# Kernel tuning notes

Measured on AMD Instinct MI355X. Metric: run time of the kernel, lower is better.

The kernel has to match this reference:

```python
import jax, jax.numpy as jnp
import numpy as np

T = 4096       # sentence length
E = 256        # embedding_dim
H = 512        # hidden_dim (bidirectional total)
HD = H // 2    # per-direction hidden
V = 100000     # vocab_size
NT = 16        # tagset_size
START, STOP = 14, 15
NEG = -10000.0


def setup_inputs() -> dict:
    key = jax.random.key(0)
    ks = jax.random.split(key, 20)
    sentence = jax.random.randint(ks[0], (T,), 0, V)
    emb = jax.random.normal(ks[1], (V, E), dtype=jnp.float32)
    # PyTorch LSTM params: gate order [i, f, g, o], weight_ih [4*HD, E], weight_hh [4*HD, HD]
    s = 1.0 / np.sqrt(HD)
    def U(k, shape):
        return jax.random.uniform(k, shape, dtype=jnp.float32, minval=-s, maxval=s)
    Wih_f, Whh_f = U(ks[2], (4 * HD, E)), U(ks[3], (4 * HD, HD))
    bih_f, bhh_f = U(ks[4], (4 * HD,)), U(ks[5], (4 * HD,))
    Wih_b, Whh_b = U(ks[6], (4 * HD, E)), U(ks[7], (4 * HD, HD))
    bih_b, bhh_b = U(ks[8], (4 * HD,)), U(ks[9], (4 * HD,))
    h0 = jax.random.normal(ks[10], (2, 1, HD), dtype=jnp.float32)  # init_hidden()
    c0 = jax.random.normal(ks[11], (2, 1, HD), dtype=jnp.float32)
    # attention params (zeros in the original; small randn for a non-degenerate baseline)
    w_omega = jax.random.normal(ks[12], (H, H), dtype=jnp.float32) * 0.01
    u_omega = jax.random.normal(ks[13], (H,), dtype=jnp.float32) * 0.01
    sl = 1.0 / np.sqrt(H)
    W_tag = jax.random.uniform(ks[14], (NT, H), dtype=jnp.float32, minval=-sl, maxval=sl)
    b_tag = jax.random.uniform(ks[15], (NT,), dtype=jnp.float32, minval=-sl, maxval=sl)
    transitions = jax.random.normal(ks[16], (NT, NT), dtype=jnp.float32)
    transitions = transitions.at[START, :].set(NEG).at[:, STOP].set(NEG)
    return dict(sentence=sentence, emb=emb,
                Wih_f=Wih_f, Whh_f=Whh_f, bih_f=bih_f, bhh_f=bhh_f,
                Wih_b=Wih_b, Whh_b=Whh_b, bih_b=bih_b, bhh_b=bhh_b,
                h0=h0, c0=c0, w_omega=w_omega, u_omega=u_omega,
                W_tag=W_tag, b_tag=b_tag, transitions=transitions)


def _lstm_dir(x, h0, c0, Wih, Whh, bih, bhh, reverse):
    # x: [T, E]; returns hidden states [T, HD]
    def step(carry, xt):
        h, c = carry
        g = xt @ Wih.T + h @ Whh.T + bih + bhh  # [4*HD]
        i, f, gg, o = jnp.split(g, 4)
        i, f, o = jax.nn.sigmoid(i), jax.nn.sigmoid(f), jax.nn.sigmoid(o)
        c = f * c + i * jnp.tanh(gg)
        h = o * jnp.tanh(c)
        return (h, c), h
    _, hs = jax.lax.scan(step, (h0, c0), x, reverse=reverse)
    return hs


def _lstm_feats(sentence, emb, Wih_f, Whh_f, bih_f, bhh_f,
                Wih_b, Whh_b, bih_b, bhh_b, h0, c0,
                w_omega, u_omega, W_tag, b_tag):
    x = emb[sentence]  # [T, E]
    hf = _lstm_dir(x, h0[0, 0], c0[0, 0], Wih_f, Whh_f, bih_f, bhh_f, False)
    hb = _lstm_dir(x, h0[1, 0], c0[1, 0], Wih_b, Whh_b, bih_b, bhh_b, True)
    out = jnp.concatenate([hf, hb], axis=-1)  # [T, H] (lstm_out with batch=1 squeezed)
    # attention_net: softmax over time of a scalar score per position
    logits = jnp.tanh(out @ w_omega) @ u_omega  # [T]
    alphas = jax.nn.softmax(logits)
    attn_out = out * alphas[:, None]  # [T, H]
    return attn_out @ W_tag.T + b_tag  # [T, NT]


def _viterbi(feats, transitions):
    init = jnp.full((NT,), NEG, dtype=feats.dtype).at[START].set(0.0)
    def step(fv, feat):
        scores = fv[None, :] + transitions  # [next_tag, prev_tag]
        bp = jnp.argmax(scores, axis=1)
        return jnp.max(scores, axis=1) + feat, bp
    fv, bps = jax.lax.scan(step, init, feats)
    terminal = fv + transitions[STOP]
    best = jnp.argmax(terminal)
    score = terminal[best]
    def back(tag, bp):
        return bp[tag], tag
    _, path = jax.lax.scan(back, best, bps, reverse=True)  # path[t] = best tag at t
    return score, path


def reference(sentence, emb, Wih_f, Whh_f, bih_f, bhh_f,
              Wih_b, Whh_b, bih_b, bhh_b, h0, c0,
              w_omega, u_omega, W_tag, b_tag, transitions):
    feats = _lstm_feats(sentence, emb, Wih_f, Whh_f, bih_f, bhh_f,
                        Wih_b, Whh_b, bih_b, bhh_b, h0, c0,
                        w_omega, u_omega, W_tag, b_tag)
    score, path = _viterbi(feats, transitions)
    return score, path
```

## Files before the change

kernel.cpp:

```cpp
#include <hip/hip_runtime.h>
#include <hip/hip_fp16.h>

#define T_LEN 4096
#define START_TAG 14
#define STOP_TAG 15
#define NEG_VAL -10000.0f

typedef unsigned int u32;
typedef unsigned short u16;
typedef unsigned long long u64;
typedef int v4i __attribute__((ext_vector_type(4)));

#define GX_OFF      0u
#define OUT_OFF     16777216u
#define LOGITS_OFF  25165824u
#define ALPHAS_OFF  25182208u
#define FEATS_OFF   25198592u
#define CMAT_OFF    25460736u
#define VIN_OFF     25591808u
#define BP_OFF      25600000u
#define BMAP_OFF    25632768u
#define STAIL_OFF   25640960u
#define BEST_OFF    25649152u

__device__ __forceinline__ u32 packq(int q0, int q1, int q2, int q3) {
  return (u32)(q0 & 255) | ((u32)(q1 & 255) << 8) |
         ((u32)(q2 & 255) << 16) | ((u32)(q3 & 255) << 24);
}

__device__ __forceinline__ float sigm(float x) {
  return __builtin_amdgcn_rcpf(1.f + __expf(-x));
}
__device__ __forceinline__ float tanh_fast(float x) {
  float e = __expf(-2.f * fabsf(x));
  float r = (1.f - e) * __builtin_amdgcn_rcpf(1.f + e);
  return copysignf(r, x);
}

#if defined(__has_builtin)
#  if __has_builtin(__builtin_amdgcn_sdot4)
#    define DOT4(a, b, c) __builtin_amdgcn_sdot4((a), (b), (c), false)
#  endif
#endif
#ifndef DOT4
__device__ __forceinline__ int dot4_emu(int a, int b, int c) {
  #pragma unroll
  for (int j = 0; j < 4; ++j)
    c += (int)((signed char)(a >> (8 * j))) * (int)((signed char)(b >> (8 * j)));
  return c;
}
#  define DOT4(a, b, c) dot4_emu((a), (b), (c))
#endif

__device__ __forceinline__ void wg_barrier() {
  asm volatile("s_waitcnt lgkmcnt(0)" ::: "memory");
  __builtin_amdgcn_s_barrier();
  __builtin_amdgcn_sched_barrier(0);
}

__global__ void prep_kernel(float* logits) {
  const int i = threadIdx.x + blockIdx.x * 1024;
  if (i < 4096) logits[i] = 0.f;
}

__global__ __launch_bounds__(256) void gx_kernel(
    const int* __restrict__ sentence, const float* __restrict__ emb,
    const float* __restrict__ Wih_f, const float* __restrict__ Wih_b,
    const float* __restrict__ bih_f, const float* __restrict__ bhh_f,
    const float* __restrict__ bih_b, const float* __restrict__ bhh_b,
    __half* __restrict__ Gx)
{
  __shared__ float ws[32][260];
  const int r0 = blockIdx.x * 32;
  const int t0 = blockIdx.y * 32;
  const int tid = threadIdx.x;
  {
    const int c4 = (tid & 63) * 4;
    const int rA = tid >> 6;
    #pragma unroll
    for (int p = 0; p < 8; ++p) {
      const int rr = rA + p * 4;
      const int R = r0 + rr;
      const float* src = (R < 1024) ? (Wih_f + (size_t)R * 256 + c4)
                                    : (Wih_b + (size_t)(R - 1024) * 256 + c4);
      *(float4*)&ws[rr][c4] = *(const float4*)src;
    }
  }
  __syncthreads();
  const int ttb = tid >> 4, rgb = tid & 15;
  const int s0r = sentence[t0 + ttb];
  const int s1r = sentence[t0 + ttb + 16];
  const float* x0p = emb + (size_t)s0r * 256;
  const float* x1p = emb + (size_t)s1r * 256;
  float acc00 = 0, acc01 = 0, acc10 = 0, acc11 = 0;
  #pragma unroll 4
  for (int c4 = 0; c4 < 256; c4 += 4) {
    float4 x0 = *(const float4*)(x0p + c4);
    float4 x1 = *(const float4*)(x1p + c4);
    float4 w0 = *(const float4*)&ws[rgb][c4];
    float4 w1 = *(const float4*)&ws[rgb + 16][c4];
    acc00 += x0.x*w0.x + x0.y*w0.y + x0.z*w0.z + x0.w*w0.w;
    acc01 += x0.x*w1.x + x0.y*w1.y + x0.z*w1.z + x0.w*w1.w;
    acc10 += x1.x*w0.x + x1.y*w0.y + x1.z*w0.z + x1.w*w0.w;
    acc11 += x1.x*w1.x + x1.y*w1.y + x1.z*w1.z + x1.w*w1.w;
  }
  #pragma unroll
  for (int ri = 0; ri < 2; ++ri) {
    const int R = r0 + rgb + ri * 16;
    const int dir = R >> 10, grow = R & 1023;
    const int gate = grow >> 8, dd = grow & 255;
    const float bias = dir ? (bih_b[grow] + bhh_b[grow])
                           : (bih_f[grow] + bhh_f[grow]);
    const float a0 = ri ? acc01 : acc00;
    const float a1 = ri ? acc11 : acc10;
    const size_t off = (size_t)dir * 1024 + dd * 4 + gate;
    Gx[(size_t)(t0 + ttb) * 2048 + off]      = __float2half(a0 + bias);
    Gx[(size_t)(t0 + ttb + 16) * 2048 + off] = __float2half(a1 + bias);
  }
}

__global__ __launch_bounds__(512, 2) void lstm_kernel(
    const float* __restrict__ Whh_f, const float* __restrict__ Whh_b,
    const float* __restrict__ h0, const float* __restrict__ c0,
    const __half* __restrict__ Gx, float* __restrict__ out_lstm)
{
  const int dir = blockIdx.x;
  const int tid = threadIdx.x;
  const int w = tid >> 6, l = tid & 63;
  const float* Whh = dir ? Whh_b : Whh_f;

  __shared__ __align__(16) char hq8[2][256];
  __shared__ __align__(16) int graw[512];
  __shared__ float fsh[512];
  __shared__ __align__(16) u16 hist[128 * 256];

  if (w < 4) {
    const int mr = l & 15, q = l >> 4;
    v4i wfrag[8][4];
    #pragma unroll
    for (int m = 0; m < 8; ++m) {
      const int row = 128 * w + 16 * m + mr;
      const float* wr = Whh + (size_t)row * 256 + 16 * q;
      float mx = 1e-10f;
      #pragma unroll
      for (int t = 0; t < 4; ++t) {
        #pragma unroll
        for (int c4 = 0; c4 < 4; ++c4) {
          float4 f = *(const float4*)(wr + 64 * t + 4 * c4);
          mx = fmaxf(mx, fmaxf(fmaxf(fabsf(f.x), fabsf(f.y)),
                               fmaxf(fabsf(f.z), fabsf(f.w))));
        }
      }
      mx = fmaxf(mx, __shfl_xor(mx, 16));
      mx = fmaxf(mx, __shfl_xor(mx, 32));
      const float qs = 127.f / mx;
      if (q == 0) fsh[row] = mx * (1.f / (127.f * 32.f));
      #pragma unroll
      for (int t = 0; t < 4; ++t) {
        u32 pk[4];
        #pragma unroll
        for (int c4 = 0; c4 < 4; ++c4) {
          float4 f = *(const float4*)(wr + 64 * t + 4 * c4);
          pk[c4] = packq((int)rintf(f.x * qs), (int)rintf(f.y * qs),
                         (int)rintf(f.z * qs), (int)rintf(f.w * qs));
        }
        v4i v; v[0] = (int)pk[0]; v[1] = (int)pk[1]; v[2] = (int)pk[2]; v[3] = (int)pk[3];
        wfrag[m][t] = v;
      }
    }
    wg_barrier();

    for (int s = 0; s < T_LEN; ++s) {
      const char* hc = hq8[s & 1];
      v4i bfr[4];
      #pragma unroll
      for (int t = 0; t < 4; ++t)
        bfr[t] = *(const v4i*)(hc + 64 * t + 16 * q);
      #pragma unroll
      for (int m = 0; m < 8; ++m) {
        v4i acc; acc[0] = 0; acc[1] = 0; acc[2] = 0; acc[3] = 0;
        acc = __builtin_amdgcn_mfma_i32_16x16x64_i8(wfrag[m][0], bfr[0], acc, 0, 0, 0);
        acc = __builtin_amdgcn_mfma_i32_16x16x64_i8(wfrag[m][1], bfr[1], acc, 0, 0, 0);
        acc = __builtin_amdgcn_mfma_i32_16x16x64_i8(wfrag[m][2], bfr[2], acc, 0, 0, 0);
        acc = __builtin_amdgcn_mfma_i32_16x16x64_i8(wfrag[m][3], bfr[3], acc, 0, 0, 0);
        if (mr == 0)
          *(v4i*)&graw[128 * w + 16 * m + 4 * q] = acc;
      }
      wg_barrier();
      wg_barrier();
      if ((s & 127) == 127) {
        const int sbase = s - 127;
        #pragma unroll 4
        for (int i = 0; i < 16; ++i) {
          const int idx = tid + i * 512;
          const int step = idx >> 6, d0 = (idx & 63) * 4;
          const int tt = sbase + step;
          const int tg = dir ? (T_LEN - 1 - tt) : tt;
          uint2 hv = ((const uint2*)hist)[idx];
          float4 ov4;
          ov4.x = __half2float(__ushort_as_half((u16)(hv.x & 0xffff)));
          ov4.y = __half2float(__ushort_as_half((u16)(hv.x >> 16)));
          ov4.z = __half2float(__ushort_as_half((u16)(hv.y & 0xffff)));
          ov4.w = __half2float(__ushort_as_half((u16)(hv.y >> 16)));
          *(float4*)&out_lstm[(size_t)tg * 512 + dir * 256 + d0] = ov4;
        }
        wg_barrier();
      }
    }
  } else {
    const int d = tid & 255;
    int wq2[2][64];
    float fsg = 0.f, fso = 0.f;
    #pragma unroll
    for (int g = 0; g < 2; ++g) {
      const float* wr = Whh + (size_t)((2 + g) * 256 + d) * 256;
      float mx = 1e-10f;
      #pragma unroll
      for (int c4 = 0; c4 < 64; ++c4) {
        float4 f = *(const float4*)(wr + c4 * 4);
        mx = fmaxf(mx, fmaxf(fmaxf(fabsf(f.x), fabsf(f.y)),
                             fmaxf(fabsf(f.z), fabsf(f.w))));
      }
      const float qs = 127.f / mx;
      const float sc = mx * (1.f / (127.f * 32.f));
      if (g == 0) fsg = sc; else fso = sc;
      #pragma unroll
      for (int c4 = 0; c4 < 64; ++c4) {
        float4 f = *(const float4*)(wr + c4 * 4);
        wq2[g][c4] = (int)packq((int)rintf(f.x * qs), (int)rintf(f.y * qs),
                                (int)rintf(f.z * qs), (int)rintf(f.w * qs));
      }
    }
    float creg = c0[dir * 256 + d];
    {
      float hv = h0[dir * 256 + d];
      int qq = max(-127, min(127, (int)rintf(hv * 32.f)));
      hq8[0][d] = (char)qq;
    }
    wg_barrier();

    const float fsi = fsh[d], fsf = fsh[256 + d];
    const uint2* Gx2 = (const uint2*)Gx;
    uint2 ga[8];
    #pragma unroll
    for (int k = 0; k < 8; ++k) {
      const int t = dir ? (T_LEN - 1 - k) : k;
      ga[k] = Gx2[(size_t)t * 512 + dir * 256 + d];
    }

    for (int sb = 0; sb < T_LEN; sb += 8) {
      uint2 gn[8];
      const bool more = (sb + 8) < T_LEN;
      if (more) {
        #pragma unroll
        for (int k = 0; k < 8; ++k) {
          const int t2 = sb + 8 + k;
          const int t = dir ? (T_LEN - 1 - t2) : t2;
          gn[k] = Gx2[(size_t)t * 512 + dir * 256 + d];
        }
      }
      #pragma unroll
      for (int k = 0; k < 8; ++k) {
        const int s = sb + k;
        const int4* hc4 = (const int4*)hq8[s & 1];
        int ag0 = 0, ag1 = 0, ao0 = 0, ao1 = 0;
        #pragma unroll
        for (int c = 0; c < 16; ++c) {
          const int4 h4 = hc4[c];
          ag0 = DOT4(wq2[0][4*c+0], h4.x, ag0);
          ao0 = DOT4(wq2[1][4*c+0], h4.x, ao0);
          ag1 = DOT4(wq2[0][4*c+1], h4.y, ag1);
          ao1 = DOT4(wq2[1][4*c+1], h4.y, ao1);
          ag0 = DOT4(wq2[0][4*c+2], h4.z, ag0);
          ao0 = DOT4(wq2[1][4*c+2], h4.z, ao0);
          ag1 = DOT4(wq2[0][4*c+3], h4.w, ag1);
          ao1 = DOT4(wq2[1][4*c+3], h4.w, ao1);
        }
        const int ag = ag0 + ag1, ao = ao0 + ao1;
        wg_barrier();
        const int ri = graw[d], rf = graw[256 + d];
        const float xi = (float)ri * fsi + __half2float(__ushort_as_half((u16)(ga[k].x & 0xffff)));
        const float xf = (float)rf * fsf + __half2float(__ushort_as_half((u16)(ga[k].x >> 16)));
        const float xg = (float)ag * fsg + __half2float(__ushort_as_half((u16)(ga[k].y & 0xffff)));
        const float xo = (float)ao * fso + __half2float(__ushort_as_half((u16)(ga[k].y >> 16)));
        const float iv = sigm(xi);
        const float fv = sigm(xf);
        const float gv = tanh_fast(xg);
        const float ov = sigm(xo);
        creg = __builtin_fmaf(fv, creg, iv * gv);
        const float h = ov * tanh_fast(creg);
        {
          int qq = max(-127, min(127, (int)rintf(h * 32.f)));
          hq8[(s + 1) & 1][d] = (char)qq;
        }
        hist[(s & 127) * 256 + d] = __half_as_ushort(__float2half(h));
        wg_barrier();
      }
      if ((sb & 127) == 120) {
        const int sbase = sb - 120;
        #pragma unroll 4
        for (int i = 0; i < 16; ++i) {
          const int idx = tid + i * 512;
          const int step = idx >> 6, d0 = (idx & 63) * 4;
          const int tt = sbase + step;
          const int tg = dir ? (T_LEN - 1 - tt) : tt;
          uint2 hv = ((const uint2*)hist)[idx];
          float4 ov4;
          ov4.x = __half2float(__ushort_as_half((u16)(hv.x & 0xffff)));
          ov4.y = __half2float(__ushort_as_half((u16)(hv.x >> 16)));
          ov4.z = __half2float(__ushort_as_half((u16)(hv.y & 0xffff)));
          ov4.w = __half2float(__ushort_as_half((u16)(hv.y >> 16)));
          *(float4*)&out_lstm[(size_t)tg * 512 + dir * 256 + d0] = ov4;
        }
        wg_barrier();
      }
      if (more) {
        #pragma unroll
        for (int k = 0; k < 8; ++k) ga[k] = gn[k];
      }
    }
  }
}

__global__ __launch_bounds__(256) void attn_kernel(
    const float* __restrict__ out_lstm, const float* __restrict__ w_omega,
    const float* __restrict__ u_omega, float* __restrict__ logits)
{
  __shared__ float bst[32][132];
  const int c0 = blockIdx.x * 32;
  const int t0 = blockIdx.y * 32;
  const int tid = threadIdx.x;
  const int ttb = tid >> 4, cgb = tid & 15;
  const float* a0p = out_lstm + (size_t)(t0 + ttb) * 512;
  const float* a1p = out_lstm + (size_t)(t0 + ttb + 16) * 512;
  float acc00 = 0, acc01 = 0, acc10 = 0, acc11 = 0;
  for (int kh = 0; kh < 4; ++kh) {
    __syncthreads();
    {
      const int cc = tid & 31;
      const int kA = tid >> 5;
      #pragma unroll
      for (int p = 0; p < 16; ++p) {
        const int kkx = kA + p * 8;
        bst[cc][kkx] = w_omega[(size_t)(kh * 128 + kkx) * 512 + c0 + cc];
      }
    }
    __syncthreads();
    #pragma unroll 4
    for (int k4 = 0; k4 < 128; k4 += 4) {
      float4 a0 = *(const float4*)(a0p + kh * 128 + k4);
      float4 a1 = *(const float4*)(a1p + kh * 128 + k4);
      float4 b0 = *(const float4*)&bst[cgb][k4];
      float4 b1 = *(const float4*)&bst[cgb + 16][k4];
      acc00 += a0.x*b0.x + a0.y*b0.y + a0.z*b0.z + a0.w*b0.w;
      acc01 += a0.x*b1.x + a0.y*b1.y + a0.z*b1.z + a0.w*b1.w;
      acc10 += a1.x*b0.x + a1.y*b0.y + a1.z*b0.z + a1.w*b0.w;
      acc11 += a1.x*b1.x + a1.y*b1.y + a1.z*b1.z + a1.w*b1.w;
    }
  }
  const float u0 = u_omega[c0 + cgb], u1 = u_omega[c0 + 16 + cgb];
  float s0 = tanh_fast(acc00) * u0 + tanh_fast(acc01) * u1;
  float s1 = tanh_fast(acc10) * u0 + tanh_fast(acc11) * u1;
  #pragma unroll
  for (int msk = 1; msk < 16; msk <<= 1) {
    s0 += __shfl_xor(s0, msk);
    s1 += __shfl_xor(s1, msk);
  }
  if (cgb == 0) {
    atomicAdd(&logits[t0 + ttb], s0);
    atomicAdd(&logits[t0 + ttb + 16], s1);
  }
}

__global__ __launch_bounds__(1024) void softmax_kernel(
    const float* __restrict__ logits, float* __restrict__ alphas)
{
  __shared__ float red[1024];
  const int tid = threadIdx.x;
  float l0 = logits[tid], l1 = logits[1024 + tid];
  float l2 = logits[2048 + tid], l3 = logits[3072 + tid];
  red[tid] = fmaxf(fmaxf(l0, l1), fmaxf(l2, l3));
  __syncthreads();
  for (int s = 512; s > 0; s >>= 1) {
    if (tid < s) red[tid] = fmaxf(red[tid], red[tid + s]);
    __syncthreads();
  }
  const float gm = red[0];
  __syncthreads();
  float e0 = __expf(l0 - gm), e1 = __expf(l1 - gm);
  float e2 = __expf(l2 - gm), e3 = __expf(l3 - gm);
  red[tid] = e0 + e1 + e2 + e3;
  __syncthreads();
  for (int s = 512; s > 0; s >>= 1) {
    if (tid < s) red[tid] += red[tid + s];
    __syncthreads();
  }
  const float inv = 1.0f / red[0];
  alphas[tid] = e0 * inv; alphas[1024 + tid] = e1 * inv;
  alphas[2048 + tid] = e2 * inv; alphas[3072 + tid] = e3 * inv;
}

__global__ __launch_bounds__(256) void feats_kernel(
    const float* __restrict__ out_lstm, const float* __restrict__ W_tag,
    const float* __restrict__ b_tag, const float* __restrict__ alphas,
    float* __restrict__ feats)
{
  __shared__ float wt[16][516];
  const int t0 = blockIdx.x * 16;
  const int tid = threadIdx.x;
  {
    const int k4 = (tid & 127) * 4;
    const int gA = tid >> 7;
    #pragma unroll
    for (int p = 0; p < 8; ++p) {
      const int tg = gA + p * 2;
      *(float4*)&wt[tg][k4] = *(const float4*)(W_tag + (size_t)tg * 512 + k4);
    }
  }
  __syncthreads();
  const int tt = tid >> 4, tg = tid & 15;
  const float* ap = out_lstm + (size_t)(t0 + tt) * 512;
  float acc = 0.f;
  #pragma unroll 4
  for (int k4 = 0; k4 < 512; k4 += 4) {
    float4 a = *(const float4*)(ap + k4);
    float4 b = *(const float4*)&wt[tg][k4];
    acc += a.x*b.x + a.y*b.y + a.z*b.z + a.w*b.w;
  }
  feats[(size_t)(t0 + tt) * 16 + tg] = acc * alphas[t0 + tt] + b_tag[tg];
}

__global__ __launch_bounds__(256) void vit_block_mats(
    const float* __restrict__ feats, const float* __restrict__ trans,
    float* __restrict__ Cmat)
{
  __shared__ float C[2][16][17];
  const int b = blockIdx.x;
  const int tid = threadIdx.x;
  const int n = tid >> 4, p = tid & 15;
  float tr[16];
  #pragma unroll
  for (int k = 0; k < 16; ++k) tr[k] = trans[n * 16 + k];
  const int t0 = b * 32;
  C[0][n][p] = tr[p] + feats[t0 * 16 + n];
  float fnext = feats[(t0 + 1) * 16 + n];
  __syncthreads();
  for (int s = 1; s < 32; ++s) {
    const float ft = fnext;
    if (s + 1 < 32) fnext = feats[(t0 + s + 1) * 16 + n];
    const int pr = (s - 1) & 1, cu = s & 1;
    float m = tr[0] + C[pr][0][p];
    #pragma unroll
    for (int k = 1; k < 16; ++k) m = fmaxf(m, tr[k] + C[pr][k][p]);
    C[cu][n][p] = m + ft;
    __syncthreads();
  }
  Cmat[b * 256 + n * 16 + p] = C[1][n][p];
}

__global__ __launch_bounds__(64) void vit_scan(
    const float* __restrict__ Cmat, const float* __restrict__ trans,
    float* __restrict__ v_in, float* __restrict__ d_out, u32* __restrict__ best_ws)
{
  const int l = threadIdx.x;
  const int n = l & 15, pg = l >> 4;
  float v = (n == START_TAG) ? 0.f : NEG_VAL;
  for (int b = 0; b < 128; ++b) {
    if (pg == 0) v_in[b * 16 + n] = v;
    float4 c4 = *(const float4*)&Cmat[b * 256 + n * 16 + pg * 4];
    float cand = c4.x + __shfl(v, pg * 4 + 0);
    cand = fmaxf(cand, c4.y + __shfl(v, pg * 4 + 1));
    cand = fmaxf(cand, c4.z + __shfl(v, pg * 4 + 2));
    cand = fmaxf(cand, c4.w + __shfl(v, pg * 4 + 3));
    cand = fmaxf(cand, __shfl_xor(cand, 16));
    cand = fmaxf(cand, __shfl_xor(cand, 32));
    v = cand;
  }
  float term = v + trans[STOP_TAG * 16 + n];
  int mi = n;
  #pragma unroll
  for (int msk = 1; msk < 16; msk <<= 1) {
    float om = __shfl_xor(term, msk); int omi = __shfl_xor(mi, msk);
    if (om > term || (om == term && omi < mi)) { term = om; mi = omi; }
  }
  if (l == 0) { d_out[0] = term; *best_ws = (u32)mi; }
}

__global__ __launch_bounds__(64) void vit_bp(
    const float* __restrict__ feats, const float* __restrict__ trans,
    const float* __restrict__ v_in, u32* __restrict__ bp)
{
  const int b = blockIdx.x;
  const int l = threadIdx.x;
  const int n = l & 15, pg = l >> 4;
  const float4 tr4 = *(const float4*)&trans[n * 16 + pg * 4];
  float v = v_in[b * 16 + n];
  const int t0 = b * 32;
  float fcur = feats[t0 * 16 + n];
  for (int s = 0; s < 32; ++s) {
    const int t = t0 + s;
    float fnext = (s + 1 < 32) ? feats[(t + 1) * 16 + n] : 0.f;
    float f0 = __shfl(v, pg * 4 + 0), f1 = __shfl(v, pg * 4 + 1);
    float f2 = __shfl(v, pg * 4 + 2), f3 = __shfl(v, pg * 4 + 3);
    float m = f0 + tr4.x; int mi = pg * 4;
    float c;
    c = f1 + tr4.y; if (c > m) { m = c; mi = pg * 4 + 1; }
    c = f2 + tr4.z; if (c > m) { m = c; mi = pg * 4 + 2; }
    c = f3 + tr4.w; if (c > m) { m = c; mi = pg * 4 + 3; }
    float om; int omi;
    om = __shfl_xor(m, 16); omi = __shfl_xor(mi, 16);
    if (om > m || (om == m && omi < mi)) { m = om; mi = omi; }
    om = __shfl_xor(m, 32); omi = __shfl_xor(mi, 32);
    if (om > m || (om == m && omi < mi)) { m = om; mi = omi; }
    u32 w = (l < 16) ? ((u32)mi << ((n & 7) * 4)) : 0u;
    w |= __shfl_xor(w, 1); w |= __shfl_xor(w, 2); w |= __shfl_xor(w, 4);
    if (l == 0) bp[t * 2] = w;
    if (l == 8) bp[t * 2 + 1] = w;
    v = m + fcur;
    fcur = fnext;
  }
}

__global__ __launch_bounds__(64) void vit_bmap(
    const u32* __restrict__ bp, u32* __restrict__ Bmap)
{
  const int b = blockIdx.x;
  const int l = threadIdx.x;
  if (l >= 16) return;
  int t = b * 32 + 31;
  u32 lo = bp[t * 2], hi = bp[t * 2 + 1];
  int A = (int)(((l < 8 ? lo : hi) >> ((l & 7) * 4)) & 15u);
  for (t = b * 32 + 30; t >= b * 32; --t) {
    lo = bp[t * 2]; hi = bp[t * 2 + 1];
    A = (int)(((A < 8 ? lo : hi) >> ((A & 7) * 4)) & 15u);
  }
  Bmap[b * 16 + l] = (u32)A;
}

__global__ __launch_bounds__(64) void vit_suffix(
    const u32* __restrict__ Bmap, u32* __restrict__ Stail)
{
  __shared__ u32 bm[2048];
  const int l = threadIdx.x;
  for (int i = l; i < 2048; i += 64) bm[i] = Bmap[i];
  __syncthreads();
  if (l < 16) {
    int S = l;
    for (int b = 127; b >= 0; --b) {
      Stail[b * 16 + l] = (u32)S;
      S = (int)bm[b * 16 + S];
    }
  }
}

__global__ __launch_bounds__(64) void vit_emit(
    const u32* __restrict__ bp, const u32* __restrict__ Stail,
    const u32* __restrict__ best_ws, float* __restrict__ d_out)
{
  const int b = blockIdx.x;
  const int l = threadIdx.x;
  const int best = (int)*best_ws;
  int A = (l < 16) ? (int)Stail[b * 16 + l] : 0;
  for (int s = 31; s >= 0; --s) {
    const int t = b * 32 + s;
    const int pv = __shfl(A, best);
    if (l == 0) d_out[1 + t] = (float)pv;
    if (s > 0) {
      const u32 lo = bp[t * 2], hi = bp[t * 2 + 1];
      A = (int)(((A < 8 ? lo : hi) >> ((A & 7) * 4)) & 15u);
    }
  }
}

extern "C" void kernel_launch(void* const* d_in, const int* in_sizes, int n_in,
                              void* d_out, int out_size, void* d_ws, size_t ws_size,
                              hipStream_t stream)
{
  const int*   sentence = (const int*)  d_in[0];
  const float* emb      = (const float*)d_in[1];
  const float* Wih_f    = (const float*)d_in[2];
  const float* Whh_f    = (const float*)d_in[3];
  const float* bih_f    = (const float*)d_in[4];
  const float* bhh_f    = (const float*)d_in[5];
  const float* Wih_b    = (const float*)d_in[6];
  const float* Whh_b    = (const float*)d_in[7];
  const float* bih_b    = (const float*)d_in[8];
  const float* bhh_b    = (const float*)d_in[9];
  const float* h0       = (const float*)d_in[10];
  const float* c0       = (const float*)d_in[11];
  const float* w_omega  = (const float*)d_in[12];
  const float* u_omega  = (const float*)d_in[13];
  const float* W_tag    = (const float*)d_in[14];
  const float* b_tag    = (const float*)d_in[15];
  const float* trans    = (const float*)d_in[16];

  char* ws = (char*)d_ws;
  __half* Gx      = (__half*)(ws + GX_OFF);
  float* out_lstm = (float*)(ws + OUT_OFF);
  float* logits   = (float*)(ws + LOGITS_OFF);
  float* alphas   = (float*)(ws + ALPHAS_OFF);
  float* feats    = (float*)(ws + FEATS_OFF);
  float* Cmat     = (float*)(ws + CMAT_OFF);
  float* v_in     = (float*)(ws + VIN_OFF);
  u32*   bp       = (u32*)  (ws + BP_OFF);
  u32*   Bmap     = (u32*)  (ws + BMAP_OFF);
  u32*   Stail    = (u32*)  (ws + STAIL_OFF);
  u32*   best_ws  = (u32*)  (ws + BEST_OFF);
  float* out      = (float*)d_out;

  hipLaunchKernelGGL(prep_kernel, dim3(4), dim3(1024), 0, stream, logits);
  hipLaunchKernelGGL(gx_kernel, dim3(64, 128), dim3(256), 0, stream,
                     sentence, emb, Wih_f, Wih_b, bih_f, bhh_f, bih_b, bhh_b, Gx);
  hipLaunchKernelGGL(lstm_kernel, dim3(2), dim3(512), 0, stream,
                     Whh_f, Whh_b, h0, c0, Gx, out_lstm);
  hipLaunchKernelGGL(attn_kernel, dim3(16, 128), dim3(256), 0, stream,
                     out_lstm, w_omega, u_omega, logits);
  hipLaunchKernelGGL(softmax_kernel, dim3(1), dim3(1024), 0, stream, logits, alphas);
  hipLaunchKernelGGL(feats_kernel, dim3(256), dim3(256), 0, stream,
                     out_lstm, W_tag, b_tag, alphas, feats);
  hipLaunchKernelGGL(vit_block_mats, dim3(128), dim3(256), 0, stream,
                     feats, trans, Cmat);
  hipLaunchKernelGGL(vit_scan, dim3(1), dim3(64), 0, stream,
                     Cmat, trans, v_in, out, best_ws);
  hipLaunchKernelGGL(vit_bp, dim3(128), dim3(64), 0, stream,
                     feats, trans, v_in, bp);
  hipLaunchKernelGGL(vit_bmap, dim3(128), dim3(64), 0, stream, bp, Bmap);
  hipLaunchKernelGGL(vit_suffix, dim3(1), dim3(64), 0, stream, Bmap, Stail);
  hipLaunchKernelGGL(vit_emit, dim3(128), dim3(64), 0, stream,
                     bp, Stail, best_ws, out);
}
```

Measured before the change: 3.968 ms.

## Move cell update into MFMA waves, exchanging only g/o gate activations via LDS

The MFMA waves now keep the i/f gate results in registers by remapping weight rows so each lane extracts its own hidden unit's i and f accumulators, and they perform the cell/hidden update themselves. The dot-product waves compute the g and o activations and publish them through shared memory instead of the MFMA waves publishing raw i/f sums. This removes the graw write-back and moves the nonlinearity work off the serial critical path, balancing work between wave groups while keeping two barriers per step. It adds register-select overhead and per-lane Gx prefetching in the MFMA waves.

```diff
diff --git a/kernel.cpp b/kernel.cpp
--- a/kernel.cpp
+++ b/kernel.cpp
@@ -130,16 +130,18 @@
   const float* Whh = dir ? Whh_b : Whh_f;
 
   __shared__ __align__(16) char hq8[2][256];
-  __shared__ __align__(16) int graw[512];
+  __shared__ __align__(8) float govt[512];
   __shared__ float fsh[512];
   __shared__ __align__(16) u16 hist[128 * 256];
+
+  const uint2* Gx2 = (const uint2*)Gx;
 
   if (w < 4) {
     const int mr = l & 15, q = l >> 4;
     v4i wfrag[8][4];
     #pragma unroll
     for (int m = 0; m < 8; ++m) {
-      const int row = 128 * w + 16 * m + mr;
+      const int row = (m >> 2) * 256 + 64 * w + 16 * (m & 3) + mr;
       const float* wr = Whh + (size_t)row * 256 + 16 * q;
       float mx = 1e-10f;
       #pragma unroll
@@ -168,28 +170,81 @@
         wfrag[m][t] = v;
       }
     }
+    const int tb = mr & 3, rgx = mr >> 2;
+    const int d = 64 * w + 16 * tb + 4 * q + rgx;
+    float creg = c0[dir * 256 + d];
+    {
+      float hv = h0[dir * 256 + d];
+      int qq = max(-127, min(127, (int)rintf(hv * 32.f)));
+      hq8[0][d] = (char)qq;
+    }
     wg_barrier();
-
-    for (int s = 0; s < T_LEN; ++s) {
-      const char* hc = hq8[s & 1];
-      v4i bfr[4];
+    const float fs0 = fsh[d], fs1 = fsh[256 + d];
+
+    uint2 ga[8];
+    #pragma unroll
+    for (int k = 0; k < 8; ++k) {
+      const int t = dir ? (T_LEN - 1 - k) : k;
+      ga[k] = Gx2[(size_t)t * 512 + dir * 256 + d];
+    }
+
+    for (int sb = 0; sb < T_LEN; sb += 8) {
+      uint2 gn[8];
+      const bool more = (sb + 8) < T_LEN;
+      if (more) {
+        #pragma unroll
+        for (int k = 0; k < 8; ++k) {
+          const int t2 = sb + 8 + k;
+          const int t = dir ? (T_LEN - 1 - t2) : t2;
+          gn[k] = Gx2[(size_t)t * 512 + dir * 256 + d];
+        }
+      }
       #pragma unroll
-      for (int t = 0; t < 4; ++t)
-        bfr[t] = *(const v4i*)(hc + 64 * t + 16 * q);
-      #pragma unroll
-      for (int m = 0; m < 8; ++m) {
-        v4i acc; acc[0] = 0; acc[1] = 0; acc[2] = 0; acc[3] = 0;
-        acc = __builtin_amdgcn_mfma_i32_16x16x64_i8(wfrag[m][0], bfr[0], acc, 0, 0, 0);
-        acc = __builtin_amdgcn_mfma_i32_16x16x64_i8(wfrag[m][1], bfr[1], acc, 0, 0, 0);
-        acc = __builtin_amdgcn_mfma_i32_16x16x64_i8(wfrag[m][2], bfr[2], acc, 0, 0, 0);
-        acc = __builtin_amdgcn_mfma_i32_16x16x64_i8(wfrag[m][3], bfr[3], acc, 0, 0, 0);
-        if (mr == 0)
-          *(v4i*)&graw[128 * w + 16 * m + 4 * q] = acc;
-      }
-      wg_barrier();
-      wg_barrier();
-      if ((s & 127) == 127) {
-        const int sbase = s - 127;
+      for (int k = 0; k < 8; ++k) {
+        const int s = sb + k;
+        const char* hc = hq8[s & 1];
+        v4i bfr[4];
+        #pragma unroll
+        for (int t = 0; t < 4; ++t)
+          bfr[t] = *(const v4i*)(hc + 64 * t + 16 * q);
+        v4i acc[8];
+        #pragma unroll
+        for (int m = 0; m < 8; ++m) {
+          v4i a; a[0] = 0; a[1] = 0; a[2] = 0; a[3] = 0;
+          a = __builtin_amdgcn_mfma_i32_16x16x64_i8(wfrag[m][0], bfr[0], a, 0, 0, 0);
+          a = __builtin_amdgcn_mfma_i32_16x16x64_i8(wfrag[m][1], bfr[1], a, 0, 0, 0);
+          a = __builtin_amdgcn_mfma_i32_16x16x64_i8(wfrag[m][2], bfr[2], a, 0, 0, 0);
+          a = __builtin_amdgcn_mfma_i32_16x16x64_i8(wfrag[m][3], bfr[3], a, 0, 0, 0);
+          acc[m] = a;
+        }
+        int e[8];
+        #pragma unroll
+        for (int m = 0; m < 8; ++m) {
+          const int elo = (rgx & 1) ? acc[m][1] : acc[m][0];
+          const int ehi = (rgx & 1) ? acc[m][3] : acc[m][2];
+          e[m] = (rgx & 2) ? ehi : elo;
+        }
+        const int i01 = (tb & 1) ? e[1] : e[0];
+        const int i23 = (tb & 1) ? e[3] : e[2];
+        const int ri  = (tb & 2) ? i23 : i01;
+        const int f01 = (tb & 1) ? e[5] : e[4];
+        const int f23 = (tb & 1) ? e[7] : e[6];
+        const int rf  = (tb & 2) ? f23 : f01;
+        const float xi = (float)ri * fs0 + __half2float(__ushort_as_half((u16)(ga[k].x & 0xffff)));
+        const float xf = (float)rf * fs1 + __half2float(__ushort_as_half((u16)(ga[k].x >> 16)));
+        const float iv = sigm(xi);
+        const float fv = sigm(xf);
+        wg_barrier();
+        const float2 go = *(const float2*)&govt[2 * d];
+        creg = __builtin_fmaf(fv, creg, iv * go.x);
+        const float h = go.y * tanh_fast(creg);
+        int qq = max(-127, min(127, (int)rintf(h * 32.f)));
+        hq8[(s + 1) & 1][d] = (char)qq;
+        hist[(s & 127) * 256 + d] = __half_as_ushort(__float2half(h));
+        wg_barrier();
+      }
+      if ((sb & 127) == 120) {
+        const int sbase = sb - 120;
         #pragma unroll 4
         for (int i = 0; i < 16; ++i) {
           const int idx = tid + i * 512;
@@ -206,9 +261,13 @@
         }
         wg_barrier();
       }
+      if (more) {
+        #pragma unroll
+        for (int k = 0; k < 8; ++k) ga[k] = gn[k];
+      }
     }
   } else {
-    const int d = tid & 255;
+    const int d = 64 * (w - 4) + l;
     int wq2[2][64];
     float fsg = 0.f, fso = 0.f;
     #pragma unroll
@@ -231,16 +290,8 @@
                                 (int)rintf(f.z * qs), (int)rintf(f.w * qs));
       }
     }
-    float creg = c0[dir * 256 + d];
-    {
-      float hv = h0[dir * 256 + d];
-      int qq = max(-127, min(127, (int)rintf(hv * 32.f)));
-      hq8[0][d] = (char)qq;
-    }
     wg_barrier();
 
-    const float fsi = fsh[d], fsf = fsh[256 + d];
-    const uint2* Gx2 = (const uint2*)Gx;
     uint2 ga[8];
     #pragma unroll
     for (int k = 0; k < 8; ++k) {
@@ -277,23 +328,13 @@
           ao1 = DOT4(wq2[1][4*c+3], h4.w, ao1);
         }
         const int ag = ag0 + ag1, ao = ao0 + ao1;
-        wg_barrier();
-        const int ri = graw[d], rf = graw[256 + d];
-        const float xi = (float)ri * fsi + __half2float(__ushort_as_half((u16)(ga[k].x & 0xffff)));
-        const float xf = (float)rf * fsf + __half2float(__ushort_as_half((u16)(ga[k].x >> 16)));
         const float xg = (float)ag * fsg + __half2float(__ushort_as_half((u16)(ga[k].y & 0xffff)));
         const float xo = (float)ao * fso + __half2float(__ushort_as_half((u16)(ga[k].y >> 16)));
-        const float iv = sigm(xi);
-        const float fv = sigm(xf);
-        const float gv = tanh_fast(xg);
-        const float ov = sigm(xo);
-        creg = __builtin_fmaf(fv, creg, iv * gv);
-        const float h = ov * tanh_fast(creg);
-        {
-          int qq = max(-127, min(127, (int)rintf(h * 32.f)));
-          hq8[(s + 1) & 1][d] = (char)qq;
-        }
-        hist[(s & 127) * 256 + d] = __half_as_ushort(__float2half(h));
+        float2 go;
+        go.x = tanh_fast(xg);
+        go.y = sigm(xo);
+        *(float2*)&govt[2 * d] = go;
+        wg_barrier();
         wg_barrier();
       }
       if ((sb & 127) == 120) {
```

Measured after the change: 4.882 ms. 23.0% more time.
